# Performance work log

Hardware: AMD Instinct MI355X
Metric: run time of the kernel (lower is better)

Reference implementation:

```python
import jax, jax.numpy as jnp
import numpy as np

B, L, H, NH = 2, 512, 128, 2
DH = H // NH
POS_VOCAB, REL_VOCAB = 512, 257


def setup_inputs() -> dict:
    key = jax.random.key(0)
    ks = jax.random.split(key, 16)
    s = 0.02
    inp = {
        "query": jax.random.normal(ks[0], (B, L, H), jnp.float32),
        "key": jax.random.normal(ks[1], (B, L, H), jnp.float32),
        "value": jax.random.normal(ks[2], (B, L, H), jnp.float32),
        "Wq": jax.random.normal(ks[3], (H, H), jnp.float32) * s,
        "bq": jnp.zeros((H,), jnp.float32),
        "Wk": jax.random.normal(ks[4], (H, H), jnp.float32) * s,
        "bk": jnp.zeros((H,), jnp.float32),
        "Wv": jax.random.normal(ks[5], (H, H), jnp.float32) * s,
        "bv": jnp.zeros((H,), jnp.float32),
        "Wo": jax.random.normal(ks[6], (H, H), jnp.float32) * s,
        "bo": jnp.zeros((H,), jnp.float32),
        "E_PK": jax.random.normal(ks[7], (POS_VOCAB, H), jnp.float32) * s,
        "E_PV": jax.random.normal(ks[8], (POS_VOCAB, H), jnp.float32) * s,
        "E_RK": jax.random.normal(ks[9], (REL_VOCAB, H), jnp.float32) * s,
        "E_RV": jax.random.normal(ks[10], (REL_VOCAB, H), jnp.float32) * s,
        "poss_seq": jax.random.randint(ks[11], (B, L), 0, POS_VOCAB),
        "interval_seq": jax.random.randint(ks[12], (B, L, L), 0, REL_VOCAB),
        # causal mask (True = attend), same role as attn_mask in the torch module
        "attn_mask": jnp.broadcast_to(jnp.tril(jnp.ones((L, L), bool)), (B, L, L)),
    }
    return inp


def reference(query, key, value, Wq, bq, Wk, bk, Wv, bv, Wo, bo,
              E_PK, E_PV, E_RK, E_RV, poss_seq, interval_seq, attn_mask):
    b, l, _ = query.shape
    # linear projections (torch Linear: x @ W.T + b)
    Q = query @ Wq.T + bq
    K = key @ Wk.T + bk + E_PK[poss_seq]
    V = value @ Wv.T + bv + E_PV[poss_seq]
    # relative key/value embeddings: (b, l, l, h, dh) -> (b, h, l, l, dh)
    rel_k = E_RK[interval_seq].reshape(b, l, l, NH, DH).transpose(0, 3, 1, 2, 4)
    rel_v = E_RV[interval_seq].reshape(b, l, l, NH, DH).transpose(0, 3, 1, 2, 4)
    # split heads: (b, h, l, dh)
    Qh = Q.reshape(b, l, NH, DH).transpose(0, 2, 1, 3)
    Kh = K.reshape(b, l, NH, DH).transpose(0, 2, 1, 3)
    Vh = V.reshape(b, l, NH, DH).transpose(0, 2, 1, 3)
    scores = jnp.einsum('bhld,bhkd->bhlk', Qh, Kh)
    scores = scores + jnp.einsum('bhld,bhlkd->bhlk', Qh, rel_k)
    scores = scores / jnp.sqrt(jnp.float32(DH))
    m = attn_mask[:, None]  # (b, 1, l, l)
    scores = jnp.where(m, scores, -jnp.inf)
    w = jax.nn.softmax(scores, axis=-1)
    w = jnp.where(m, w, 0.0)
    out = jnp.einsum('bhlk,bhkd->bhld', w, Vh)
    out = out + jnp.einsum('bhlk,bhlkd->bhld', w, rel_v)
    out = out.transpose(0, 2, 1, 3).reshape(b, l, H)
    out = out @ Wo.T + bo
    out = jnp.where(jnp.isnan(out), 0.0, out)
    return out
```

## Files before the change

### kernel.cpp

```cpp
#include <hip/hip_runtime.h>
#include <math.h>

#define LL 512
#define HH 128
#define NHH 2
#define DHH 64
#define RELV 257
#define PKS  260

#define OFF_QH   0
#define OFF_KT   131072
#define OFF_VH   262144
#define OFF_PK   393216
#define OFF_WQT  925696
#define OFF_WKT  942080
#define OFF_WVT  958464
#define OFF_WOT  974848
#define OFF_ERKT 991232

__global__ void prep_kernel(const float* Wq, const float* Wk, const float* Wv,
                            const float* Wo, const float* E_RK, float* ws) {
    int g = blockIdx.x * 256 + threadIdx.x;
    if (g < 65536) {
        int m = g >> 14, rem = g & 16383, i = rem >> 7, j = rem & 127;
        const float* W = (m == 0) ? Wq : (m == 1) ? Wk : (m == 2) ? Wv : Wo;
        ws[OFF_WQT + m * 16384 + i * 128 + j] = W[j * 128 + i];
    } else if (g < 65536 + 128 * RELV) {
        int g2 = g - 65536;
        int hd = g2 / RELV, r = g2 - hd * RELV;
        ws[OFF_ERKT + hd * RELV + r] = E_RK[r * HH + hd];
    }
}

__launch_bounds__(256)
__global__ void qkv_kernel(const float* q_in, const float* k_in, const float* v_in,
                           const float* bq, const float* bk, const float* bv,
                           const float* E_PK, const float* E_PV, const int* poss,
                           const float* Wqt, const float* Wkt, const float* Wvt,
                           const float* ERKt,
                           float* Qh, float* Kt, float* Vh, float* PK) {
    int row0 = blockIdx.x * 2;
    int b = row0 >> 9;
    int l0 = row0 & 511;
    int t = threadIdx.x;

    __shared__ float xin[3][2][128];
    __shared__ float pp[3][2][2][128];
    __shared__ float qr[2][128];

    for (int g = t; g < 768; g += 256) {
        int m = g >> 8, rem = g & 255, rr = rem >> 7, i = rem & 127;
        const float* src = (m == 0) ? q_in : (m == 1) ? k_in : v_in;
        xin[m][rr][i] = src[(row0 + rr) * 128 + i];
    }
    __syncthreads();

    int j = t & 127, half = t >> 7;
    float aq0 = 0, ak0 = 0, av0 = 0, aq1 = 0, ak1 = 0, av1 = 0;
    int i0 = half * 64;
#pragma unroll 8
    for (int i = i0; i < i0 + 64; i++) {
        float wq = Wqt[i * 128 + j], wk = Wkt[i * 128 + j], wv = Wvt[i * 128 + j];
        aq0 += xin[0][0][i] * wq; aq1 += xin[0][1][i] * wq;
        ak0 += xin[1][0][i] * wk; ak1 += xin[1][1][i] * wk;
        av0 += xin[2][0][i] * wv; av1 += xin[2][1][i] * wv;
    }
    pp[0][0][half][j] = aq0; pp[0][1][half][j] = aq1;
    pp[1][0][half][j] = ak0; pp[1][1][half][j] = ak1;
    pp[2][0][half][j] = av0; pp[2][1][half][j] = av1;
    __syncthreads();

    {
        int rr = t >> 7;
        int row = row0 + rr, l = l0 + rr;
        int pos = poss[row];
        float q = pp[0][rr][0][j] + pp[0][rr][1][j] + bq[j];
        float k = pp[1][rr][0][j] + pp[1][rr][1][j] + bk[j] + E_PK[pos * 128 + j];
        float v = pp[2][rr][0][j] + pp[2][rr][1][j] + bv[j] + E_PV[pos * 128 + j];
        int h = j >> 6, d = j & 63, bh = b * NHH + h;
        Qh[(bh * LL + l) * DHH + d] = q;
        Vh[(bh * LL + l) * DHH + d] = v;
        Kt[(bh * DHH + d) * LL + l] = k;
        qr[rr][j] = q;
    }
    __syncthreads();

    int h = t >> 7, rl = t & 127;
    const float* qh0 = qr[0] + h * 64;
    const float* qh1 = qr[1] + h * 64;
    const float* erb = ERKt + h * 64 * RELV;
    float* pk0 = PK + ((b * NHH + h) * LL + l0) * PKS;
    float* pk1 = pk0 + PKS;
#pragma unroll
    for (int pass = 0; pass < 3; pass++) {
        int r = rl + pass * 128;
        if (r < RELV) {
            float a0 = 0.f, a1 = 0.f;
#pragma unroll 8
            for (int dd = 0; dd < 64; dd++) {
                float er = erb[dd * RELV + r];
                a0 += qh0[dd] * er; a1 += qh1[dd] * er;
            }
            pk0[r] = a0; pk1[r] = a1;
        }
    }
}

__launch_bounds__(512)
__global__ void attn_kernel(const float* Qh, const float* Kt, const float* Vh,
                            const float* PK, const float* E_RV,
                            const float* Wot, const float* bo,
                            const int* interval, float* out) {
    int blk = blockIdx.x;
    int b = blk & 1;
    int l = 511 - (blk >> 1);
    int t = threadIdx.x;
    int w = t >> 6, lane = t & 63;
    int h = w >> 2, s = w & 3;
    int bh = b * NHH + h;
    int nk = l + 1;
    int kstep = (((nk + 3) >> 2) + 1) & ~1;
    int kbase = s * kstep; if (kbase > nk) kbase = nk;
    int kend = kbase + kstep; if (kend > nk) kend = nk;

    __shared__ float q2[2][DHH];
    __shared__ __align__(16) float pks[2][PKS];
    __shared__ float wb[2][RELV];
    __shared__ __align__(8) float sc[8][128];
    __shared__ float oa[8][DHH];
    __shared__ float ao[HH];
    __shared__ float po[4][HH];
    __shared__ float reds[8];

    if (t < 128) {
        int hh = t >> 6, dd = t & 63;
        q2[hh][dd] = Qh[((b * NHH + hh) * LL + l) * DHH + dd];
    }
    if (t < 130) {
        int hh = t >= 65;
        int c = t - hh * 65;
        const float4* src = (const float4*)(PK + ((b * NHH + hh) * LL + l) * PKS);
        ((float4*)pks[hh])[c] = src[c];
    }
    for (int idx = t; idx < 2 * RELV; idx += 512) {
        int hh = idx >= RELV;
        wb[hh][idx - hh * RELV] = 0.f;
    }
    __syncthreads();

    int k0 = kbase + lane * 2;
    const int* idxr = interval + (b * LL + l) * LL;
    float ax = 0.f, ay = 0.f;
    int2 i2 = make_int2(0, 0);
    if (k0 < kend) {
        i2 = *(const int2*)(idxr + k0);
        const float* kb = Kt + bh * DHH * LL + k0;
#pragma unroll 16
        for (int d = 0; d < DHH; d++) {
            float2 kk = *(const float2*)(kb + d * LL);
            float qd = q2[h][d];
            ax += qd * kk.x; ay += qd * kk.y;
        }
    }
    float e0 = (k0 + 0 < kend) ? __expf((ax + pks[h][i2.x]) * 0.125f) : 0.f;
    float e1 = (k0 + 1 < kend) ? __expf((ay + pks[h][i2.y]) * 0.125f) : 0.f;

    float ssum = e0 + e1;
#pragma unroll
    for (int off = 32; off > 0; off >>= 1) ssum += __shfl_down(ssum, off);
    if (lane == 0) reds[w] = ssum;

    *(float2*)&sc[w][lane * 2] = make_float2(e0, e1);
    if (k0 + 0 < kend) atomicAdd(&wb[h][i2.x], e0);
    if (k0 + 1 < kend) atomicAdd(&wb[h][i2.y], e1);
    __syncthreads();

    float acc0 = 0.f, acc1 = 0.f, acc2 = 0.f, acc3 = 0.f;
    const float* vb = Vh + bh * LL * DHH + lane;
    int kcnt = kend - kbase; if (kcnt < 0) kcnt = 0;
    int niter = (kcnt + 3) >> 2;
    for (int ci = 0; ci < niter; ci++) {
        int k = kbase + ci * 4;
        const float* scw = sc[w] + ci * 4;
        acc0 += scw[0] * vb[(k + 0) * DHH];
        acc1 += scw[1] * vb[(k + 1) * DHH];
        acc2 += scw[2] * vb[(k + 2) * DHH];
        acc3 += scw[3] * vb[(k + 3) * DHH];
    }

    {
        int r0 = s * 64;
        const float* ev = E_RV + h * 64 + lane;
        const float* wbh = wb[h];
#pragma unroll 4
        for (int rr = 0; rr < 64; rr += 4) {
            int r = r0 + rr;
            acc0 += wbh[r + 0] * ev[(r + 0) * HH];
            acc1 += wbh[r + 1] * ev[(r + 1) * HH];
            acc2 += wbh[r + 2] * ev[(r + 2) * HH];
            acc3 += wbh[r + 3] * ev[(r + 3) * HH];
        }
        if (s == 3) acc0 += wbh[256] * ev[256 * HH];
    }

    float inv = 1.f / (((reds[h * 4 + 0] + reds[h * 4 + 1]) +
                        (reds[h * 4 + 2] + reds[h * 4 + 3])));
    oa[w][lane] = ((acc0 + acc1) + (acc2 + acc3)) * inv;
    __syncthreads();

    if (t < 128) {
        int hh = t >> 6, dd = t & 63;
        ao[t] = (oa[hh * 4 + 0][dd] + oa[hh * 4 + 1][dd]) +
                (oa[hh * 4 + 2][dd] + oa[hh * 4 + 3][dd]);
    }
    __syncthreads();

    int j = t & 127, iq = t >> 7;
    float pa = 0.f, pb = 0.f;
    int ib = iq * 32;
#pragma unroll 8
    for (int ii = 0; ii < 32; ii += 2) {
        pa += ao[ib + ii]     * Wot[(ib + ii) * HH + j];
        pb += ao[ib + ii + 1] * Wot[(ib + ii + 1) * HH + j];
    }
    po[iq][j] = pa + pb;
    __syncthreads();
    if (t < HH) {
        float o = (po[0][t] + po[1][t]) + (po[2][t] + po[3][t]) + bo[t];
        if (isnan(o)) o = 0.f;
        out[(b * LL + l) * HH + t] = o;
    }
}

extern "C" void kernel_launch(void* const* d_in, const int* in_sizes, int n_in,
                              void* d_out, int out_size, void* d_ws, size_t ws_size,
                              hipStream_t stream) {
    const float* query = (const float*)d_in[0];
    const float* key   = (const float*)d_in[1];
    const float* value = (const float*)d_in[2];
    const float* Wq = (const float*)d_in[3];  const float* bq = (const float*)d_in[4];
    const float* Wk = (const float*)d_in[5];  const float* bk = (const float*)d_in[6];
    const float* Wv = (const float*)d_in[7];  const float* bv = (const float*)d_in[8];
    const float* Wo = (const float*)d_in[9];  const float* bo = (const float*)d_in[10];
    const float* E_PK = (const float*)d_in[11];
    const float* E_PV = (const float*)d_in[12];
    const float* E_RK = (const float*)d_in[13];
    const float* E_RV = (const float*)d_in[14];
    const int* poss     = (const int*)d_in[15];
    const int* interval = (const int*)d_in[16];

    float* ws = (float*)d_ws;
    float* Qh   = ws + OFF_QH;
    float* Kt   = ws + OFF_KT;
    float* Vh   = ws + OFF_VH;
    float* PK   = ws + OFF_PK;
    float* Wqt  = ws + OFF_WQT;
    float* Wkt  = ws + OFF_WKT;
    float* Wvt  = ws + OFF_WVT;
    float* Wot  = ws + OFF_WOT;
    float* ERKt = ws + OFF_ERKT;
    float* out = (float*)d_out;

    prep_kernel<<<385, 256, 0, stream>>>(Wq, Wk, Wv, Wo, E_RK, ws);
    qkv_kernel<<<512, 256, 0, stream>>>(query, key, value, bq, bk, bv,
                                        E_PK, E_PV, poss, Wqt, Wkt, Wvt, ERKt,
                                        Qh, Kt, Vh, PK);
    attn_kernel<<<1024, 512, 0, stream>>>(Qh, Kt, Vh, PK, E_RV, Wot, bo,
                                          interval, out);
}
```

Before: 142.5 us.

## Process two query rows per attention block and four rows per QKV block

The attention kernel now handles two adjacent query rows per block, so K, V, E_RV and Wo loads are shared between both rows and the grid is halved. The QKV projection kernel processes four rows per 512-thread block, reusing each weight and E_RK load across four rows. This cuts redundant global and L2 traffic per row, at the cost of more registers and shared memory per block and fewer blocks in flight.

After: 130.9 us. 8.2% less time.

```diff
diff --git a/kernel.cpp b/kernel.cpp
--- a/kernel.cpp
+++ b/kernel.cpp
@@ -32,51 +32,58 @@
     }
 }
 
-__launch_bounds__(256)
+__launch_bounds__(512)
 __global__ void qkv_kernel(const float* q_in, const float* k_in, const float* v_in,
                            const float* bq, const float* bk, const float* bv,
                            const float* E_PK, const float* E_PV, const int* poss,
                            const float* Wqt, const float* Wkt, const float* Wvt,
                            const float* ERKt,
                            float* Qh, float* Kt, float* Vh, float* PK) {
-    int row0 = blockIdx.x * 2;
+    int row0 = blockIdx.x * 4;
     int b = row0 >> 9;
     int l0 = row0 & 511;
     int t = threadIdx.x;
 
-    __shared__ float xin[3][2][128];
-    __shared__ float pp[3][2][2][128];
-    __shared__ float qr[2][128];
-
-    for (int g = t; g < 768; g += 256) {
-        int m = g >> 8, rem = g & 255, rr = rem >> 7, i = rem & 127;
+    __shared__ float xin[3][4][128];
+    __shared__ float pp[3][4][4][128];
+    __shared__ float qr[4][128];
+
+    for (int g = t; g < 1536; g += 512) {
+        int m = g >> 9, rem = g & 511, rr = rem >> 7, i = rem & 127;
         const float* src = (m == 0) ? q_in : (m == 1) ? k_in : v_in;
         xin[m][rr][i] = src[(row0 + rr) * 128 + i];
     }
     __syncthreads();
 
-    int j = t & 127, half = t >> 7;
-    float aq0 = 0, ak0 = 0, av0 = 0, aq1 = 0, ak1 = 0, av1 = 0;
-    int i0 = half * 64;
+    int j = t & 127, iq = t >> 7;
+    float aq0 = 0, aq1 = 0, aq2 = 0, aq3 = 0;
+    float ak0 = 0, ak1 = 0, ak2 = 0, ak3 = 0;
+    float av0 = 0, av1 = 0, av2 = 0, av3 = 0;
+    int i0 = iq * 32;
 #pragma unroll 8
-    for (int i = i0; i < i0 + 64; i++) {
+    for (int i = i0; i < i0 + 32; i++) {
         float wq = Wqt[i * 128 + j], wk = Wkt[i * 128 + j], wv = Wvt[i * 128 + j];
         aq0 += xin[0][0][i] * wq; aq1 += xin[0][1][i] * wq;
+        aq2 += xin[0][2][i] * wq; aq3 += xin[0][3][i] * wq;
         ak0 += xin[1][0][i] * wk; ak1 += xin[1][1][i] * wk;
+        ak2 += xin[1][2][i] * wk; ak3 += xin[1][3][i] * wk;
         av0 += xin[2][0][i] * wv; av1 += xin[2][1][i] * wv;
-    }
-    pp[0][0][half][j] = aq0; pp[0][1][half][j] = aq1;
-    pp[1][0][half][j] = ak0; pp[1][1][half][j] = ak1;
-    pp[2][0][half][j] = av0; pp[2][1][half][j] = av1;
+        av2 += xin[2][2][i] * wv; av3 += xin[2][3][i] * wv;
+    }
+    pp[0][0][iq][j] = aq0; pp[0][1][iq][j] = aq1; pp[0][2][iq][j] = aq2; pp[0][3][iq][j] = aq3;
+    pp[1][0][iq][j] = ak0; pp[1][1][iq][j] = ak1; pp[1][2][iq][j] = ak2; pp[1][3][iq][j] = ak3;
+    pp[2][0][iq][j] = av0; pp[2][1][iq][j] = av1; pp[2][2][iq][j] = av2; pp[2][3][iq][j] = av3;
     __syncthreads();
 
     {
         int rr = t >> 7;
         int row = row0 + rr, l = l0 + rr;
         int pos = poss[row];
-        float q = pp[0][rr][0][j] + pp[0][rr][1][j] + bq[j];
-        float k = pp[1][rr][0][j] + pp[1][rr][1][j] + bk[j] + E_PK[pos * 128 + j];
-        float v = pp[2][rr][0][j] + pp[2][rr][1][j] + bv[j] + E_PV[pos * 128 + j];
+        float q = (pp[0][rr][0][j] + pp[0][rr][1][j]) + (pp[0][rr][2][j] + pp[0][rr][3][j]) + bq[j];
+        float k = (pp[1][rr][0][j] + pp[1][rr][1][j]) + (pp[1][rr][2][j] + pp[1][rr][3][j]) + bk[j]
+                  + E_PK[pos * 128 + j];
+        float v = (pp[2][rr][0][j] + pp[2][rr][1][j]) + (pp[2][rr][2][j] + pp[2][rr][3][j]) + bv[j]
+                  + E_PV[pos * 128 + j];
         int h = j >> 6, d = j & 63, bh = b * NHH + h;
         Qh[(bh * LL + l) * DHH + d] = q;
         Vh[(bh * LL + l) * DHH + d] = v;
@@ -85,24 +92,23 @@
     }
     __syncthreads();
 
-    int h = t >> 7, rl = t & 127;
-    const float* qh0 = qr[0] + h * 64;
-    const float* qh1 = qr[1] + h * 64;
-    const float* erb = ERKt + h * 64 * RELV;
-    float* pk0 = PK + ((b * NHH + h) * LL + l0) * PKS;
-    float* pk1 = pk0 + PKS;
-#pragma unroll
-    for (int pass = 0; pass < 3; pass++) {
-        int r = rl + pass * 128;
-        if (r < RELV) {
-            float a0 = 0.f, a1 = 0.f;
+    for (int idx = t; idx < 2 * RELV; idx += 512) {
+        int h = idx >= RELV;
+        int r = idx - h * RELV;
+        const float* er = ERKt + h * 64 * RELV + r;
+        const float* q0 = qr[0] + h * 64;
+        const float* q1 = qr[1] + h * 64;
+        const float* q2v = qr[2] + h * 64;
+        const float* q3 = qr[3] + h * 64;
+        float a0 = 0.f, a1 = 0.f, a2 = 0.f, a3 = 0.f;
 #pragma unroll 8
-            for (int dd = 0; dd < 64; dd++) {
-                float er = erb[dd * RELV + r];
-                a0 += qh0[dd] * er; a1 += qh1[dd] * er;
-            }
-            pk0[r] = a0; pk1[r] = a1;
+        for (int dd = 0; dd < 64; dd++) {
+            float e = er[dd * RELV];
+            a0 += q0[dd] * e; a1 += q1[dd] * e;
+            a2 += q2v[dd] * e; a3 += q3[dd] * e;
         }
+        float* pk = PK + ((b * NHH + h) * LL + l0) * PKS + r;
+        pk[0] = a0; pk[PKS] = a1; pk[2 * PKS] = a2; pk[3 * PKS] = a3;
     }
 }
 
@@ -113,122 +119,155 @@
                             const int* interval, float* out) {
     int blk = blockIdx.x;
     int b = blk & 1;
-    int l = 511 - (blk >> 1);
+    int p = blk >> 1;
+    int l0 = 510 - 2 * p;
+    int nk0 = l0 + 1, nk1 = l0 + 2;
     int t = threadIdx.x;
     int w = t >> 6, lane = t & 63;
     int h = w >> 2, s = w & 3;
     int bh = b * NHH + h;
-    int nk = l + 1;
-    int kstep = (((nk + 3) >> 2) + 1) & ~1;
-    int kbase = s * kstep; if (kbase > nk) kbase = nk;
-    int kend = kbase + kstep; if (kend > nk) kend = nk;
-
-    __shared__ float q2[2][DHH];
-    __shared__ __align__(16) float pks[2][PKS];
-    __shared__ float wb[2][RELV];
-    __shared__ __align__(8) float sc[8][128];
-    __shared__ float oa[8][DHH];
-    __shared__ float ao[HH];
-    __shared__ float po[4][HH];
-    __shared__ float reds[8];
-
-    if (t < 128) {
-        int hh = t >> 6, dd = t & 63;
-        q2[hh][dd] = Qh[((b * NHH + hh) * LL + l) * DHH + dd];
-    }
-    if (t < 130) {
-        int hh = t >= 65;
-        int c = t - hh * 65;
-        const float4* src = (const float4*)(PK + ((b * NHH + hh) * LL + l) * PKS);
-        ((float4*)pks[hh])[c] = src[c];
-    }
-    for (int idx = t; idx < 2 * RELV; idx += 512) {
-        int hh = idx >= RELV;
-        wb[hh][idx - hh * RELV] = 0.f;
+    int kstep = (((nk1 + 3) >> 2) + 1) & ~1;
+    int kbase = s * kstep; if (kbase > nk1) kbase = nk1;
+    int kend = kbase + kstep; if (kend > nk1) kend = nk1;
+
+    __shared__ float q2[2][2][DHH];
+    __shared__ __align__(16) float pks[2][2][PKS];
+    __shared__ float wb[2][2][RELV];
+    __shared__ __align__(8) float sc[2][8][128];
+    __shared__ float oa[2][8][DHH];
+    __shared__ float ao[2][HH];
+    __shared__ float po[2][4][HH];
+    __shared__ float reds[2][8];
+
+    if (t < 256) {
+        int row = t >> 7, hh = (t >> 6) & 1, dd = t & 63;
+        q2[row][hh][dd] = Qh[((b * NHH + hh) * LL + (l0 + row)) * DHH + dd];
+    }
+    if (t < 260) {
+        int row = t / 130, rem = t - row * 130;
+        int hh = rem / 65, c = rem - hh * 65;
+        const float4* src = (const float4*)(PK + ((b * NHH + hh) * LL + l0 + row) * PKS);
+        ((float4*)pks[row][hh])[c] = src[c];
+    }
+    {
+        float* wbf = &wb[0][0][0];
+        for (int idx = t; idx < 4 * RELV; idx += 512) wbf[idx] = 0.f;
     }
     __syncthreads();
 
     int k0 = kbase + lane * 2;
-    const int* idxr = interval + (b * LL + l) * LL;
-    float ax = 0.f, ay = 0.f;
-    int2 i2 = make_int2(0, 0);
+    const int* idxr0 = interval + (b * LL + l0) * LL;
+    const int* idxr1 = idxr0 + LL;
+    float ax0 = 0.f, ay0 = 0.f, ax1 = 0.f, ay1 = 0.f;
+    int2 i20 = make_int2(0, 0), i21 = make_int2(0, 0);
     if (k0 < kend) {
-        i2 = *(const int2*)(idxr + k0);
+        i20 = *(const int2*)(idxr0 + k0);
+        i21 = *(const int2*)(idxr1 + k0);
         const float* kb = Kt + bh * DHH * LL + k0;
 #pragma unroll 16
         for (int d = 0; d < DHH; d++) {
             float2 kk = *(const float2*)(kb + d * LL);
-            float qd = q2[h][d];
-            ax += qd * kk.x; ay += qd * kk.y;
+            float qd0 = q2[0][h][d], qd1 = q2[1][h][d];
+            ax0 += qd0 * kk.x; ay0 += qd0 * kk.y;
+            ax1 += qd1 * kk.x; ay1 += qd1 * kk.y;
         }
     }
-    float e0 = (k0 + 0 < kend) ? __expf((ax + pks[h][i2.x]) * 0.125f) : 0.f;
-    float e1 = (k0 + 1 < kend) ? __expf((ay + pks[h][i2.y]) * 0.125f) : 0.f;
-
-    float ssum = e0 + e1;
+    bool m00 = (k0 < kend) && (k0 < nk0);
+    bool m01 = (k0 + 1 < kend) && (k0 + 1 < nk0);
+    bool m10 = (k0 < kend);
+    bool m11 = (k0 + 1 < kend);
+    float e00 = m00 ? __expf((ax0 + pks[0][h][i20.x]) * 0.125f) : 0.f;
+    float e01 = m01 ? __expf((ay0 + pks[0][h][i20.y]) * 0.125f) : 0.f;
+    float e10 = m10 ? __expf((ax1 + pks[1][h][i21.x]) * 0.125f) : 0.f;
+    float e11 = m11 ? __expf((ay1 + pks[1][h][i21.y]) * 0.125f) : 0.f;
+
+    float ss0 = e00 + e01, ss1 = e10 + e11;
 #pragma unroll
-    for (int off = 32; off > 0; off >>= 1) ssum += __shfl_down(ssum, off);
-    if (lane == 0) reds[w] = ssum;
-
-    *(float2*)&sc[w][lane * 2] = make_float2(e0, e1);
-    if (k0 + 0 < kend) atomicAdd(&wb[h][i2.x], e0);
-    if (k0 + 1 < kend) atomicAdd(&wb[h][i2.y], e1);
-    __syncthreads();
-
-    float acc0 = 0.f, acc1 = 0.f, acc2 = 0.f, acc3 = 0.f;
+    for (int off = 32; off > 0; off >>= 1) {
+        ss0 += __shfl_down(ss0, off);
+        ss1 += __shfl_down(ss1, off);
+    }
+    if (lane == 0) { reds[0][w] = ss0; reds[1][w] = ss1; }
+
+    *(float2*)&sc[0][w][lane * 2] = make_float2(e00, e01);
+    *(float2*)&sc[1][w][lane * 2] = make_float2(e10, e11);
+    if (m00) atomicAdd(&wb[0][h][i20.x], e00);
+    if (m01) atomicAdd(&wb[0][h][i20.y], e01);
+    if (m10) atomicAdd(&wb[1][h][i21.x], e10);
+    if (m11) atomicAdd(&wb[1][h][i21.y], e11);
+    __syncthreads();
+
+    float a00 = 0.f, a01 = 0.f, a02 = 0.f, a03 = 0.f;
+    float a10 = 0.f, a11 = 0.f, a12 = 0.f, a13 = 0.f;
     const float* vb = Vh + bh * LL * DHH + lane;
     int kcnt = kend - kbase; if (kcnt < 0) kcnt = 0;
     int niter = (kcnt + 3) >> 2;
     for (int ci = 0; ci < niter; ci++) {
         int k = kbase + ci * 4;
-        const float* scw = sc[w] + ci * 4;
-        acc0 += scw[0] * vb[(k + 0) * DHH];
-        acc1 += scw[1] * vb[(k + 1) * DHH];
-        acc2 += scw[2] * vb[(k + 2) * DHH];
-        acc3 += scw[3] * vb[(k + 3) * DHH];
+        const float* s0 = sc[0][w] + ci * 4;
+        const float* s1 = sc[1][w] + ci * 4;
+        float v0 = vb[(k + 0) * DHH], v1 = vb[(k + 1) * DHH];
+        float v2 = vb[(k + 2) * DHH], v3 = vb[(k + 3) * DHH];
+        a00 += s0[0] * v0; a01 += s0[1] * v1; a02 += s0[2] * v2; a03 += s0[3] * v3;
+        a10 += s1[0] * v0; a11 += s1[1] * v1; a12 += s1[2] * v2; a13 += s1[3] * v3;
     }
 
     {
         int r0 = s * 64;
         const float* ev = E_RV + h * 64 + lane;
-        const float* wbh = wb[h];
+        const float* w0 = wb[0][h];
+        const float* w1 = wb[1][h];
 #pragma unroll 4
         for (int rr = 0; rr < 64; rr += 4) {
             int r = r0 + rr;
-            acc0 += wbh[r + 0] * ev[(r + 0) * HH];
-            acc1 += wbh[r + 1] * ev[(r + 1) * HH];
-            acc2 += wbh[r + 2] * ev[(r + 2) * HH];
-            acc3 += wbh[r + 3] * ev[(r + 3) * HH];
+            float ev0 = ev[(r + 0) * HH], ev1 = ev[(r + 1) * HH];
+            float ev2 = ev[(r + 2) * HH], ev3 = ev[(r + 3) * HH];
+            a00 += w0[r + 0] * ev0; a01 += w0[r + 1] * ev1;
+            a02 += w0[r + 2] * ev2; a03 += w0[r + 3] * ev3;
+            a10 += w1[r + 0] * ev0; a11 += w1[r + 1] * ev1;
+            a12 += w1[r + 2] * ev2; a13 += w1[r + 3] * ev3;
         }
-        if (s == 3) acc0 += wbh[256] * ev[256 * HH];
-    }
-
-    float inv = 1.f / (((reds[h * 4 + 0] + reds[h * 4 + 1]) +
-                        (reds[h * 4 + 2] + reds[h * 4 + 3])));
-    oa[w][lane] = ((acc0 + acc1) + (acc2 + acc3)) * inv;
-    __syncthreads();
-
-    if (t < 128) {
-        int hh = t >> 6, dd = t & 63;
-        ao[t] = (oa[hh * 4 + 0][dd] + oa[hh * 4 + 1][dd]) +
-                (oa[hh * 4 + 2][dd] + oa[hh * 4 + 3][dd]);
+        if (s == 3) {
+            float e256 = ev[256 * HH];
+            a00 += w0[256] * e256;
+            a10 += w1[256] * e256;
+        }
+    }
+
+    float inv0 = 1.f / ((reds[0][h * 4 + 0] + reds[0][h * 4 + 1]) +
+                        (reds[0][h * 4 + 2] + reds[0][h * 4 + 3]));
+    float inv1 = 1.f / ((reds[1][h * 4 + 0] + reds[1][h * 4 + 1]) +
+                        (reds[1][h * 4 + 2] + reds[1][h * 4 + 3]));
+    oa[0][w][lane] = ((a00 + a01) + (a02 + a03)) * inv0;
+    oa[1][w][lane] = ((a10 + a11) + (a12 + a13)) * inv1;
+    __syncthreads();
+
+    if (t < 256) {
+        int row = t >> 7, hd = t & 127, hh = hd >> 6, dd = hd & 63;
+        ao[row][hd] = (oa[row][hh * 4 + 0][dd] + oa[row][hh * 4 + 1][dd]) +
+                      (oa[row][hh * 4 + 2][dd] + oa[row][hh * 4 + 3][dd]);
     }
     __syncthreads();
 
     int j = t & 127, iq = t >> 7;
-    float pa = 0.f, pb = 0.f;
+    float p0a = 0.f, p0b = 0.f, p1a = 0.f, p1b = 0.f;
     int ib = iq * 32;
 #pragma unroll 8
     for (int ii = 0; ii < 32; ii += 2) {
-        pa += ao[ib + ii]     * Wot[(ib + ii) * HH + j];
-        pb += ao[ib + ii + 1] * Wot[(ib + ii + 1) * HH + j];
-    }
-    po[iq][j] = pa + pb;
-    __syncthreads();
-    if (t < HH) {
-        float o = (po[0][t] + po[1][t]) + (po[2][t] + po[3][t]) + bo[t];
+        float wv0 = Wot[(ib + ii) * HH + j];
+        float wv1 = Wot[(ib + ii + 1) * HH + j];
+        p0a += ao[0][ib + ii] * wv0; p0b += ao[0][ib + ii + 1] * wv1;
+        p1a += ao[1][ib + ii] * wv0; p1b += ao[1][ib + ii + 1] * wv1;
+    }
+    po[0][iq][j] = p0a + p0b;
+    po[1][iq][j] = p1a + p1b;
+    __syncthreads();
+    if (t < 256) {
+        int row = t >> 7, jj = t & 127;
+        float o = (po[row][0][jj] + po[row][1][jj]) +
+                  (po[row][2][jj] + po[row][3][jj]) + bo[jj];
         if (isnan(o)) o = 0.f;
-        out[(b * LL + l) * HH + t] = o;
+        out[(b * LL + l0 + row) * HH + jj] = o;
     }
 }
 
@@ -262,9 +301,9 @@
     float* out = (float*)d_out;
 
     prep_kernel<<<385, 256, 0, stream>>>(Wq, Wk, Wv, Wo, E_RK, ws);
-    qkv_kernel<<<512, 256, 0, stream>>>(query, key, value, bq, bk, bv,
+    qkv_kernel<<<256, 512, 0, stream>>>(query, key, value, bq, bk, bv,
                                         E_PK, E_PV, poss, Wqt, Wkt, Wvt, ERKt,
                                         Qh, Kt, Vh, PK);
-    attn_kernel<<<1024, 512, 0, stream>>>(Qh, Kt, Vh, PK, E_RV, Wot, bo,
-                                          interval, out);
+    attn_kernel<<<512, 512, 0, stream>>>(Qh, Kt, Vh, PK, E_RV, Wot, bo,
+                                         interval, out);
 }
```
